# Performance work log

Hardware: AMD Instinct MI355X
Metric: run time of the kernel (lower is better)

Reference implementation:

```python
import jax, jax.numpy as jnp
import numpy as np

D_MODEL = 768
MIMO_RANK = 4


def setup_inputs() -> dict:
    key = jax.random.key(0)
    ks = jax.random.split(key, 6)
    B, T, D, R = 2, 2048, D_MODEL, MIMO_RANK
    x = jax.random.normal(ks[0], (B, T, D), dtype=jnp.float32)
    norm_w = jnp.ones((D,), dtype=jnp.float32)
    W_in = jax.random.normal(ks[1], (D * R * 2, D), dtype=jnp.float32) * 0.02
    W_out = jax.random.normal(ks[2], (D, D), dtype=jnp.float32) * 0.02
    a_param = jax.random.normal(ks[3], (D, R, 2), dtype=jnp.float32) * 0.12
    b_param = jax.random.normal(ks[4], (D, R, 2), dtype=jnp.float32) * 0.15
    c_param = jax.random.normal(ks[5], (D, R, 2), dtype=jnp.float32) * 0.15
    return {"x": x, "norm_w": norm_w, "W_in": W_in, "W_out": W_out,
            "a_param": a_param, "b_param": b_param, "c_param": c_param}


def reference(x, norm_w, W_in, W_out, a_param, b_param, c_param):
    B, T, D = x.shape
    R = a_param.shape[1]
    # RMSNorm
    xn = x * jax.lax.rsqrt(jnp.mean(x * x, axis=-1, keepdims=True) + 1e-6) * norm_w
    # in_proj -> interleaved complex MIMO input u: [B,T,D,R,2]
    u = (xn @ W_in.T).reshape(B, T, D, R, 2)
    # coefficients (tanh-bounded; |a| scaled by 0.97 for stability)
    a = jnp.tanh(a_param) * 0.97
    b = jnp.tanh(b_param)
    c = jnp.tanh(c_param)
    ac = jax.lax.complex(a[..., 0], a[..., 1])  # [D,R]
    bc = jax.lax.complex(b[..., 0], b[..., 1])
    cc = jax.lax.complex(c[..., 0], c[..., 1])
    uc = jax.lax.complex(u[..., 0], u[..., 1])  # [B,T,D,R]
    # linear complex recurrence s_t = a * s_{t-1} + b * u_t, zero init state,
    # parallelized with an associative scan over time.
    bu = bc[None, None] * uc
    A = jnp.broadcast_to(ac[None, None], bu.shape)

    def comb(l, r):
        return (l[0] * r[0], r[0] * l[1] + r[1])

    _, s = jax.lax.associative_scan(comb, (A, bu), axis=1)  # [B,T,D,R] complex
    # output mix: real part of c * h, summed over MIMO rank -> [B,T,D]
    y = jnp.real(cc[None, None] * s).sum(axis=-1)
    return y @ W_out.T
```

## Files before the change

kernel.cpp:

```cpp
#include <hip/hip_runtime.h>
#include <hip/hip_bf16.h>
#include <stdint.h>

#define BATCH 2
#define TT 2048
#define DM 768
#define RR 4
#define M_TOK 4096
#define NFEAT 6144
#define NCH 6144
#define CHUNK 64
#define NCHUNK 32

typedef __attribute__((ext_vector_type(8))) short short8;
typedef __attribute__((ext_vector_type(4))) float float4v;

__device__ inline float bf2f(uint32_t bits16) {
    union { uint32_t u; float f; } x; x.u = bits16 << 16; return x.f;
}

typedef const __attribute__((address_space(1))) void* gptr_t;
typedef __attribute__((address_space(3))) void* lptr_t;

__device__ inline void async_ld16(const void* g, void* l) {
    __builtin_amdgcn_global_load_lds((gptr_t)(uintptr_t)g, (lptr_t)(uintptr_t)l,
                                     16, 0, 0);
}

__device__ inline void store_c(__hip_bfloat16* C, size_t idx, float v) {
    C[idx] = __float2bfloat16(v);
}
__device__ inline void store_c(float* C, size_t idx, float v) { C[idx] = v; }

__global__ void cast_f32_bf16(const float* __restrict__ s,
                              __hip_bfloat16* __restrict__ d, int n) {
    int i = blockIdx.x * 256 + threadIdx.x;
    if (i < n) d[i] = __float2bfloat16(s[i]);
}

__global__ void coeff_kernel(const float* __restrict__ ap,
                             const float* __restrict__ bp,
                             const float* __restrict__ cp,
                             float2* __restrict__ ac, float2* __restrict__ bc,
                             float2* __restrict__ cc, float2* __restrict__ aL) {
    int i = blockIdx.x * 256 + threadIdx.x;
    if (i >= DM * RR) return;
    float ar = tanhf(ap[2 * i])     * 0.97f;
    float ai = tanhf(ap[2 * i + 1]) * 0.97f;
    ac[i] = make_float2(ar, ai);
    bc[i] = make_float2(tanhf(bp[2 * i]), tanhf(bp[2 * i + 1]));
    cc[i] = make_float2(tanhf(cp[2 * i]), tanhf(cp[2 * i + 1]));
    float xr = ar, xi = ai;
    #pragma unroll
    for (int k = 0; k < 6; ++k) {
        float nr = xr * xr - xi * xi;
        float ni = 2.f * xr * xi;
        xr = nr; xi = ni;
    }
    aL[i] = make_float2(xr, xi);
}

__global__ __launch_bounds__(256) void rmsnorm_kernel(
    const float* __restrict__ x, const float* __restrict__ w,
    __hip_bfloat16* __restrict__ xn) {
    int row = blockIdx.x;
    const float* xr = x + (size_t)row * DM;
    int tid = threadIdx.x;
    float v0 = xr[tid], v1 = xr[tid + 256], v2 = xr[tid + 512];
    float ss = v0 * v0 + v1 * v1 + v2 * v2;
    #pragma unroll
    for (int o = 1; o < 64; o <<= 1) ss += __shfl_xor(ss, o);
    __shared__ float wsum[4];
    if ((tid & 63) == 0) wsum[tid >> 6] = ss;
    __syncthreads();
    float tot = wsum[0] + wsum[1] + wsum[2] + wsum[3];
    float scale = rsqrtf(tot * (1.f / DM) + 1e-6f);
    size_t base = (size_t)row * DM;
    xn[base + tid]       = __float2bfloat16(v0 * scale * w[tid]);
    xn[base + tid + 256] = __float2bfloat16(v1 * scale * w[tid + 256]);
    xn[base + tid + 512] = __float2bfloat16(v2 * scale * w[tid + 512]);
}

template <typename OutT>
__global__ __launch_bounds__(256) void gemm_bt(
    const __hip_bfloat16* __restrict__ A, const __hip_bfloat16* __restrict__ B,
    OutT* __restrict__ C, int M, int N, int K) {
    __shared__ __attribute__((aligned(16))) __hip_bfloat16 lA[128 * 64];
    __shared__ __attribute__((aligned(16))) __hip_bfloat16 lB[128 * 64];
    const int tid  = threadIdx.x;
    const int lane = tid & 63;
    const int wave = tid >> 6;
    const int quad = lane >> 4;
    const int l15  = lane & 15;
    const int wm = (wave >> 1) * 64;
    const int wn = (wave & 1) * 64;
    const int m0 = blockIdx.y * 128;
    const int n0 = blockIdx.x * 128;

    float4v acc[4][4] = {};

    for (int k0 = 0; k0 < K; k0 += 64) {
        __syncthreads();
        #pragma unroll
        for (int it = 0; it < 4; ++it) {
            int p = it * 256 + tid;
            int row = p >> 3;
            int cg = (p & 7) ^ (row & 7);
            async_ld16(A + (size_t)(m0 + row) * K + k0 + cg * 8, lA + p * 8);
        }
        #pragma unroll
        for (int it = 0; it < 4; ++it) {
            int p = it * 256 + tid;
            int row = p >> 3;
            int cg = (p & 7) ^ (row & 7);
            async_ld16(B + (size_t)(n0 + row) * K + k0 + cg * 8, lB + p * 8);
        }
        __syncthreads();
        #pragma unroll
        for (int s = 0; s < 2; ++s) {
            short8 af[4], bfr[4];
            #pragma unroll
            for (int i = 0; i < 4; ++i) {
                int r = wm + i * 16 + l15;
                int c = (s * 4 + quad) ^ (r & 7);
                af[i] = *(const short8*)(lA + r * 64 + c * 8);
            }
            #pragma unroll
            for (int j = 0; j < 4; ++j) {
                int r = wn + j * 16 + l15;
                int c = (s * 4 + quad) ^ (r & 7);
                bfr[j] = *(const short8*)(lB + r * 64 + c * 8);
            }
            #pragma unroll
            for (int i = 0; i < 4; ++i)
                #pragma unroll
                for (int j = 0; j < 4; ++j)
                    acc[i][j] = __builtin_amdgcn_mfma_f32_16x16x32_bf16(
                        af[i], bfr[j], acc[i][j], 0, 0, 0);
        }
    }
    #pragma unroll
    for (int i = 0; i < 4; ++i)
        #pragma unroll
        for (int j = 0; j < 4; ++j)
            #pragma unroll
            for (int rg = 0; rg < 4; ++rg) {
                int row = m0 + wm + i * 16 + quad * 4 + rg;
                int col = n0 + wn + j * 16 + l15;
                store_c(C, (size_t)row * N + col, acc[i][j][rg]);
            }
}

__global__ __launch_bounds__(256) void scan_passA(
    const uint32_t* __restrict__ u,
    const float2* __restrict__ ac, const float2* __restrict__ bc,
    float2* __restrict__ chunkEnd) {
    int c = blockIdx.x * 256 + threadIdx.x;
    int j = blockIdx.y;
    int b = c >= DM * RR;
    int rem = c - b * DM * RR;
    float2 a = ac[rem], bb = bc[rem];
    float sr = 0.f, si = 0.f;
    size_t base = ((size_t)b * TT + (size_t)j * CHUNK) * (DM * RR) + rem;
    #pragma unroll 8
    for (int i = 0; i < CHUNK; ++i) {
        uint32_t uw = u[base + (size_t)i * (DM * RR)];
        float ur = bf2f(uw & 0xffffu), ui = bf2f(uw >> 16);
        float tr = bb.x * ur - bb.y * ui;
        float ti = bb.x * ui + bb.y * ur;
        float nr = a.x * sr - a.y * si + tr;
        float ni = a.x * si + a.y * sr + ti;
        sr = nr; si = ni;
    }
    chunkEnd[(size_t)j * NCH + c] = make_float2(sr, si);
}

__global__ __launch_bounds__(256) void scan_passB(
    const float2* __restrict__ chunkEnd, const float2* __restrict__ aLp,
    float2* __restrict__ carry) {
    int c = blockIdx.x * 256 + threadIdx.x;
    int b = c >= DM * RR;
    int rem = c - b * DM * RR;
    float2 aL = aLp[rem];
    float sr = 0.f, si = 0.f;
    for (int j = 0; j < NCHUNK; ++j) {
        carry[(size_t)j * NCH + c] = make_float2(sr, si);
        float2 e = chunkEnd[(size_t)j * NCH + c];
        float nr = aL.x * sr - aL.y * si + e.x;
        float ni = aL.x * si + aL.y * sr + e.y;
        sr = nr; si = ni;
    }
}

__global__ __launch_bounds__(256) void scan_passC(
    const uint32_t* __restrict__ u,
    const float2* __restrict__ ac, const float2* __restrict__ bc,
    const float2* __restrict__ cc, const float2* __restrict__ carry,
    __hip_bfloat16* __restrict__ y) {
    int c = blockIdx.x * 256 + threadIdx.x;
    int j = blockIdx.y;
    int b = c >= DM * RR;
    int rem = c - b * DM * RR;
    int d = rem >> 2;
    float2 a = ac[rem], bb = bc[rem], cf = cc[rem];
    float2 s0 = carry[(size_t)j * NCH + c];
    float sr = s0.x, si = s0.y;
    size_t ubase = ((size_t)b * TT + (size_t)j * CHUNK) * (DM * RR) + rem;
    size_t ybase = ((size_t)b * TT + (size_t)j * CHUNK) * DM + d;
    #pragma unroll 4
    for (int i = 0; i < CHUNK; ++i) {
        uint32_t uw = u[ubase + (size_t)i * (DM * RR)];
        float ur = bf2f(uw & 0xffffu), ui = bf2f(uw >> 16);
        float tr = bb.x * ur - bb.y * ui;
        float ti = bb.x * ui + bb.y * ur;
        float nr = a.x * sr - a.y * si + tr;
        float ni = a.x * si + a.y * sr + ti;
        sr = nr; si = ni;
        float contrib = cf.x * sr - cf.y * si;
        contrib += __shfl_xor(contrib, 1);
        contrib += __shfl_xor(contrib, 2);
        if ((threadIdx.x & 3) == 0)
            y[ybase + (size_t)i * DM] = __float2bfloat16(contrib);
    }
}

extern "C" void kernel_launch(void* const* d_in, const int* in_sizes, int n_in,
                              void* d_out, int out_size, void* d_ws,
                              size_t ws_size, hipStream_t stream) {
    const float* x      = (const float*)d_in[0];
    const float* norm_w = (const float*)d_in[1];
    const float* W_in   = (const float*)d_in[2];
    const float* W_out  = (const float*)d_in[3];
    const float* a_p    = (const float*)d_in[4];
    const float* b_p    = (const float*)d_in[5];
    const float* c_p    = (const float*)d_in[6];
    float* out = (float*)d_out;

    char* ws = (char*)d_ws;
    size_t off = 0;
    auto alloc = [&](size_t bytes) {
        void* p = ws + off;
        off += (bytes + 255) & ~(size_t)255;
        return p;
    };
    __hip_bfloat16* Win_bf  = (__hip_bfloat16*)alloc((size_t)NFEAT * DM * 2);
    __hip_bfloat16* Wout_bf = (__hip_bfloat16*)alloc((size_t)DM * DM * 2);
    __hip_bfloat16* xn      = (__hip_bfloat16*)alloc((size_t)M_TOK * DM * 2);
    __hip_bfloat16* u       = (__hip_bfloat16*)alloc((size_t)M_TOK * NFEAT * 2);
    __hip_bfloat16* y       = (__hip_bfloat16*)alloc((size_t)M_TOK * DM * 2);
    float2* ac = (float2*)alloc((size_t)DM * RR * 8);
    float2* bc = (float2*)alloc((size_t)DM * RR * 8);
    float2* cc = (float2*)alloc((size_t)DM * RR * 8);
    float2* aL = (float2*)alloc((size_t)DM * RR * 8);
    float2* chunkEnd = (float2*)alloc((size_t)NCHUNK * NCH * 8);
    float2* carry    = (float2*)alloc((size_t)NCHUNK * NCH * 8);

    {
        int n1 = NFEAT * DM;
        cast_f32_bf16<<<(n1 + 255) / 256, 256, 0, stream>>>(W_in, Win_bf, n1);
        int n2 = DM * DM;
        cast_f32_bf16<<<(n2 + 255) / 256, 256, 0, stream>>>(W_out, Wout_bf, n2);
        coeff_kernel<<<(DM * RR + 255) / 256, 256, 0, stream>>>(
            a_p, b_p, c_p, ac, bc, cc, aL);
    }
    rmsnorm_kernel<<<M_TOK, 256, 0, stream>>>(x, norm_w, xn);
    gemm_bt<__hip_bfloat16><<<dim3(NFEAT / 128, M_TOK / 128), 256, 0, stream>>>(
        xn, Win_bf, u, M_TOK, NFEAT, DM);
    scan_passA<<<dim3(NCH / 256, NCHUNK), 256, 0, stream>>>(
        (const uint32_t*)u, ac, bc, chunkEnd);
    scan_passB<<<NCH / 256, 256, 0, stream>>>(chunkEnd, aL, carry);
    scan_passC<<<dim3(NCH / 256, NCHUNK), 256, 0, stream>>>(
        (const uint32_t*)u, ac, bc, cc, carry, y);
    gemm_bt<float><<<dim3(DM / 128, M_TOK / 128), 256, 0, stream>>>(
        y, Wout_bf, out, M_TOK, DM, DM);
}
```

Before: 202.8 us.

## Merge prep kernels, fold carry pass into scan, retile output GEMM

Three setup kernels (two weight casts and the coefficient kernel) become one launch. The separate carry-propagation pass is removed: each chunk block in pass C now recomputes its incoming state by serially combining the earlier chunk ends, trading a launch and the carry buffer for redundant reads and arithmetic of up to 31 chunk ends per block. The GEMM is templated on tile size, and the small output projection uses 64x64 tiles so it launches more blocks and fills more compute units.

Result: faster. 192.7 us (-5.0%).

```diff
diff --git a/kernel.cpp b/kernel.cpp
--- a/kernel.cpp
+++ b/kernel.cpp
@@ -32,32 +32,35 @@
 }
 __device__ inline void store_c(float* C, size_t idx, float v) { C[idx] = v; }
 
-__global__ void cast_f32_bf16(const float* __restrict__ s,
-                              __hip_bfloat16* __restrict__ d, int n) {
+__global__ void prep_kernel(const float* __restrict__ W_in,
+                            const float* __restrict__ W_out,
+                            const float* __restrict__ ap,
+                            const float* __restrict__ bp,
+                            const float* __restrict__ cp,
+                            __hip_bfloat16* __restrict__ Win_bf,
+                            __hip_bfloat16* __restrict__ Wout_bf,
+                            float2* __restrict__ ac, float2* __restrict__ bc,
+                            float2* __restrict__ cc, float2* __restrict__ aL) {
+    const int n1 = NFEAT * DM;
+    const int n2 = DM * DM;
     int i = blockIdx.x * 256 + threadIdx.x;
-    if (i < n) d[i] = __float2bfloat16(s[i]);
-}
-
-__global__ void coeff_kernel(const float* __restrict__ ap,
-                             const float* __restrict__ bp,
-                             const float* __restrict__ cp,
-                             float2* __restrict__ ac, float2* __restrict__ bc,
-                             float2* __restrict__ cc, float2* __restrict__ aL) {
-    int i = blockIdx.x * 256 + threadIdx.x;
-    if (i >= DM * RR) return;
-    float ar = tanhf(ap[2 * i])     * 0.97f;
-    float ai = tanhf(ap[2 * i + 1]) * 0.97f;
-    ac[i] = make_float2(ar, ai);
-    bc[i] = make_float2(tanhf(bp[2 * i]), tanhf(bp[2 * i + 1]));
-    cc[i] = make_float2(tanhf(cp[2 * i]), tanhf(cp[2 * i + 1]));
-    float xr = ar, xi = ai;
-    #pragma unroll
-    for (int k = 0; k < 6; ++k) {
-        float nr = xr * xr - xi * xi;
-        float ni = 2.f * xr * xi;
-        xr = nr; xi = ni;
-    }
-    aL[i] = make_float2(xr, xi);
+    if (i < n1) Win_bf[i] = __float2bfloat16(W_in[i]);
+    else if (i < n1 + n2) Wout_bf[i - n1] = __float2bfloat16(W_out[i - n1]);
+    if (i < DM * RR) {
+        float ar = tanhf(ap[2 * i])     * 0.97f;
+        float ai = tanhf(ap[2 * i + 1]) * 0.97f;
+        ac[i] = make_float2(ar, ai);
+        bc[i] = make_float2(tanhf(bp[2 * i]), tanhf(bp[2 * i + 1]));
+        cc[i] = make_float2(tanhf(cp[2 * i]), tanhf(cp[2 * i + 1]));
+        float xr = ar, xi = ai;
+        #pragma unroll
+        for (int k = 0; k < 6; ++k) {
+            float nr = xr * xr - xi * xi;
+            float ni = 2.f * xr * xi;
+            xr = nr; xi = ni;
+        }
+        aL[i] = make_float2(xr, xi);
+    }
 }
 
 __global__ __launch_bounds__(256) void rmsnorm_kernel(
@@ -81,35 +84,37 @@
     xn[base + tid + 512] = __float2bfloat16(v2 * scale * w[tid + 512]);
 }
 
-template <typename OutT>
+template <int BM, int BN, typename OutT>
 __global__ __launch_bounds__(256) void gemm_bt(
     const __hip_bfloat16* __restrict__ A, const __hip_bfloat16* __restrict__ B,
     OutT* __restrict__ C, int M, int N, int K) {
-    __shared__ __attribute__((aligned(16))) __hip_bfloat16 lA[128 * 64];
-    __shared__ __attribute__((aligned(16))) __hip_bfloat16 lB[128 * 64];
+    constexpr int MI = BM / 32;
+    constexpr int NJ = BN / 32;
+    __shared__ __attribute__((aligned(16))) __hip_bfloat16 lA[BM * 64];
+    __shared__ __attribute__((aligned(16))) __hip_bfloat16 lB[BN * 64];
     const int tid  = threadIdx.x;
     const int lane = tid & 63;
     const int wave = tid >> 6;
     const int quad = lane >> 4;
     const int l15  = lane & 15;
-    const int wm = (wave >> 1) * 64;
-    const int wn = (wave & 1) * 64;
-    const int m0 = blockIdx.y * 128;
-    const int n0 = blockIdx.x * 128;
-
-    float4v acc[4][4] = {};
+    const int wm = (wave >> 1) * (BM / 2);
+    const int wn = (wave & 1) * (BN / 2);
+    const int m0 = blockIdx.y * BM;
+    const int n0 = blockIdx.x * BN;
+
+    float4v acc[MI][NJ] = {};
 
     for (int k0 = 0; k0 < K; k0 += 64) {
         __syncthreads();
         #pragma unroll
-        for (int it = 0; it < 4; ++it) {
+        for (int it = 0; it < BM / 32; ++it) {
             int p = it * 256 + tid;
             int row = p >> 3;
             int cg = (p & 7) ^ (row & 7);
             async_ld16(A + (size_t)(m0 + row) * K + k0 + cg * 8, lA + p * 8);
         }
         #pragma unroll
-        for (int it = 0; it < 4; ++it) {
+        for (int it = 0; it < BN / 32; ++it) {
             int p = it * 256 + tid;
             int row = p >> 3;
             int cg = (p & 7) ^ (row & 7);
@@ -118,31 +123,31 @@
         __syncthreads();
         #pragma unroll
         for (int s = 0; s < 2; ++s) {
-            short8 af[4], bfr[4];
-            #pragma unroll
-            for (int i = 0; i < 4; ++i) {
+            short8 af[MI], bfr[NJ];
+            #pragma unroll
+            for (int i = 0; i < MI; ++i) {
                 int r = wm + i * 16 + l15;
                 int c = (s * 4 + quad) ^ (r & 7);
                 af[i] = *(const short8*)(lA + r * 64 + c * 8);
             }
             #pragma unroll
-            for (int j = 0; j < 4; ++j) {
+            for (int j = 0; j < NJ; ++j) {
                 int r = wn + j * 16 + l15;
                 int c = (s * 4 + quad) ^ (r & 7);
                 bfr[j] = *(const short8*)(lB + r * 64 + c * 8);
             }
             #pragma unroll
-            for (int i = 0; i < 4; ++i)
+            for (int i = 0; i < MI; ++i)
                 #pragma unroll
-                for (int j = 0; j < 4; ++j)
+                for (int j = 0; j < NJ; ++j)
                     acc[i][j] = __builtin_amdgcn_mfma_f32_16x16x32_bf16(
                         af[i], bfr[j], acc[i][j], 0, 0, 0);
         }
     }
     #pragma unroll
-    for (int i = 0; i < 4; ++i)
-        #pragma unroll
-        for (int j = 0; j < 4; ++j)
+    for (int i = 0; i < MI; ++i)
+        #pragma unroll
+        for (int j = 0; j < NJ; ++j)
             #pragma unroll
             for (int rg = 0; rg < 4; ++rg) {
                 int row = m0 + wm + i * 16 + quad * 4 + rg;
@@ -175,27 +180,11 @@
     chunkEnd[(size_t)j * NCH + c] = make_float2(sr, si);
 }
 
-__global__ __launch_bounds__(256) void scan_passB(
-    const float2* __restrict__ chunkEnd, const float2* __restrict__ aLp,
-    float2* __restrict__ carry) {
-    int c = blockIdx.x * 256 + threadIdx.x;
-    int b = c >= DM * RR;
-    int rem = c - b * DM * RR;
-    float2 aL = aLp[rem];
-    float sr = 0.f, si = 0.f;
-    for (int j = 0; j < NCHUNK; ++j) {
-        carry[(size_t)j * NCH + c] = make_float2(sr, si);
-        float2 e = chunkEnd[(size_t)j * NCH + c];
-        float nr = aL.x * sr - aL.y * si + e.x;
-        float ni = aL.x * si + aL.y * sr + e.y;
-        sr = nr; si = ni;
-    }
-}
-
 __global__ __launch_bounds__(256) void scan_passC(
     const uint32_t* __restrict__ u,
     const float2* __restrict__ ac, const float2* __restrict__ bc,
-    const float2* __restrict__ cc, const float2* __restrict__ carry,
+    const float2* __restrict__ cc, const float2* __restrict__ aLp,
+    const float2* __restrict__ chunkEnd,
     __hip_bfloat16* __restrict__ y) {
     int c = blockIdx.x * 256 + threadIdx.x;
     int j = blockIdx.y;
@@ -203,8 +192,15 @@
     int rem = c - b * DM * RR;
     int d = rem >> 2;
     float2 a = ac[rem], bb = bc[rem], cf = cc[rem];
-    float2 s0 = carry[(size_t)j * NCH + c];
-    float sr = s0.x, si = s0.y;
+    float2 aL = aLp[rem];
+    float sr = 0.f, si = 0.f;
+    #pragma unroll 4
+    for (int jj = 0; jj < j; ++jj) {
+        float2 e = chunkEnd[(size_t)jj * NCH + c];
+        float nr = aL.x * sr - aL.y * si + e.x;
+        float ni = aL.x * si + aL.y * sr + e.y;
+        sr = nr; si = ni;
+    }
     size_t ubase = ((size_t)b * TT + (size_t)j * CHUNK) * (DM * RR) + rem;
     size_t ybase = ((size_t)b * TT + (size_t)j * CHUNK) * DM + d;
     #pragma unroll 4
@@ -253,24 +249,21 @@
     float2* cc = (float2*)alloc((size_t)DM * RR * 8);
     float2* aL = (float2*)alloc((size_t)DM * RR * 8);
     float2* chunkEnd = (float2*)alloc((size_t)NCHUNK * NCH * 8);
-    float2* carry    = (float2*)alloc((size_t)NCHUNK * NCH * 8);
 
     {
-        int n1 = NFEAT * DM;
-        cast_f32_bf16<<<(n1 + 255) / 256, 256, 0, stream>>>(W_in, Win_bf, n1);
-        int n2 = DM * DM;
-        cast_f32_bf16<<<(n2 + 255) / 256, 256, 0, stream>>>(W_out, Wout_bf, n2);
-        coeff_kernel<<<(DM * RR + 255) / 256, 256, 0, stream>>>(
-            a_p, b_p, c_p, ac, bc, cc, aL);
+        int n_total = NFEAT * DM + DM * DM;
+        prep_kernel<<<(n_total + 255) / 256, 256, 0, stream>>>(
+            W_in, W_out, a_p, b_p, c_p, Win_bf, Wout_bf, ac, bc, cc, aL);
     }
     rmsnorm_kernel<<<M_TOK, 256, 0, stream>>>(x, norm_w, xn);
-    gemm_bt<__hip_bfloat16><<<dim3(NFEAT / 128, M_TOK / 128), 256, 0, stream>>>(
-        xn, Win_bf, u, M_TOK, NFEAT, DM);
+    gemm_bt<128, 128, __hip_bfloat16>
+        <<<dim3(NFEAT / 128, M_TOK / 128), 256, 0, stream>>>(
+            xn, Win_bf, u, M_TOK, NFEAT, DM);
     scan_passA<<<dim3(NCH / 256, NCHUNK), 256, 0, stream>>>(
         (const uint32_t*)u, ac, bc, chunkEnd);
-    scan_passB<<<NCH / 256, 256, 0, stream>>>(chunkEnd, aL, carry);
     scan_passC<<<dim3(NCH / 256, NCHUNK), 256, 0, stream>>>(
-        (const uint32_t*)u, ac, bc, cc, carry, y);
-    gemm_bt<float><<<dim3(DM / 128, M_TOK / 128), 256, 0, stream>>>(
-        y, Wout_bf, out, M_TOK, DM, DM);
-}
+        (const uint32_t*)u, ac, bc, cc, aL, chunkEnd, y);
+    gemm_bt<64, 64, float>
+        <<<dim3(DM / 64, M_TOK / 64), 256, 0, stream>>>(
+            y, Wout_bf, out, M_TOK, DM, DM);
+}
```
